# Performance work log

Hardware: AMD Instinct MI355X
Metric: run time of the kernel (lower is better)

Reference implementation:

```python
import jax, jax.numpy as jnp
import numpy as np

B, N, F, H1, H2, NC = 1024, 64, 1024, 256, 128, 128
ALPHA = 0.2   # LeakyReLU slope
BN_EPS = 1e-5


def setup_inputs() -> dict:
    key = jax.random.key(0)
    ks = jax.random.split(key, 20)
    d = {}
    d["x"] = jax.random.normal(ks[0], (B, 1, F), dtype=jnp.float32)
    d["neighbor"] = jax.random.normal(ks[1], (B, N, 1, F), dtype=jnp.float32)
    # GraphAttn layer 1 params
    d["W1"] = jax.random.normal(ks[2], (H1, F), dtype=jnp.float32) / np.sqrt(F)
    d["b1"] = jnp.zeros((H1,), dtype=jnp.float32)
    d["a11"] = jax.random.normal(ks[3], (H1,), dtype=jnp.float32) / np.sqrt(H1)
    d["a12"] = jax.random.normal(ks[4], (H1,), dtype=jnp.float32) / np.sqrt(H1)
    d["g1"] = jnp.ones((), dtype=jnp.float32)   # BatchNorm1d(1) weight (scalar)
    d["be1"] = jnp.zeros((), dtype=jnp.float32)  # BatchNorm1d(1) bias
    # GraphAttn layer 2 params
    d["W2"] = jax.random.normal(ks[5], (H2, H1), dtype=jnp.float32) / np.sqrt(H1)
    d["b2"] = jnp.zeros((H2,), dtype=jnp.float32)
    d["a21"] = jax.random.normal(ks[6], (H2,), dtype=jnp.float32) / np.sqrt(H2)
    d["a22"] = jax.random.normal(ks[7], (H2,), dtype=jnp.float32) / np.sqrt(H2)
    d["g2"] = jnp.ones((), dtype=jnp.float32)
    d["be2"] = jnp.zeros((), dtype=jnp.float32)
    # final classifier
    d["Wl"] = jax.random.normal(ks[8], (NC, H2), dtype=jnp.float32) / np.sqrt(H2)
    d["bl"] = jnp.zeros((NC,), dtype=jnp.float32)
    return d


def _l2norm_c(t):
    # torch nf.normalize default: p=2, dim=1 -> here the singleton channel axis (-2)
    n = jnp.sqrt(jnp.sum(t * t, axis=-2, keepdims=True))
    return t / jnp.maximum(n, 1e-12)


def _gat_layer(x, nb, W, b, a_self, a_nb):
    # x: [B,1,Fin], nb: [B,N,1,Fin]
    xh = jnp.einsum('bcf,hf->bch', x, W) + b        # [B,1,H]
    nbh = jnp.einsum('bncf,hf->bnch', nb, W) + b    # [B,N,1,H]
    # att1(x[i]) + att2(neighbor[i]) -> scores over N (C==1 squeezed)
    s = (jnp.einsum('bch,h->bc', xh, a_self)[:, None, :]
         + jnp.einsum('bnch,h->bnc', nbh, a_nb))[..., 0]   # [B,N]
    A = jax.nn.softmax(jax.nn.leaky_relu(s, ALPHA), axis=1)  # softmax over neighbors
    out = jnp.einsum('bn,bnch->bch', A, nbh)        # [B,1,H]
    return out, nbh


def _bn_relu(t, g, b, axes):
    # BatchNorm1d(1) in training mode: stats over all non-channel dims of the tensor
    m = jnp.mean(t, axis=axes, keepdims=True)
    v = jnp.mean(jnp.square(t - m), axis=axes, keepdims=True)
    return jax.nn.relu(g * (t - m) * jax.lax.rsqrt(v + BN_EPS) + b)


def reference(x, neighbor, W1, b1, a11, a12, g1, be1,
              W2, b2, a21, a22, g2, be2, Wl, bl):
    x = _l2norm_c(x)
    nb = _l2norm_c(neighbor)
    x, nb = _gat_layer(x, nb, W1, b1, a11, a12)
    # acvt1 applied to x [B,1,H1] (stats over B,H) and to each neighbor tensor
    # [N,1,H1] separately (per-sample stats -> axes (1,3) of [B,N,1,H1])
    x = _bn_relu(x, g1, be1, axes=(0, 2))
    nb = _bn_relu(nb, g1, be1, axes=(1, 3))
    x, nb = _gat_layer(x, nb, W2, b2, a21, a22)
    x = _bn_relu(x, g2, be2, axes=(0, 2))
    # Flatten -> Dropout(p=0) -> Linear
    logits = jnp.einsum('bh,ch->bc', x.reshape(x.shape[0], -1), Wl) + bl
    return logits
```

## Files before the change

### kernel.cpp

```cpp
#include <hip/hip_runtime.h>
#include <hip/hip_bf16.h>

#define B_    1024
#define N_    64
#define F_    1024
#define H1_   256
#define H2_   128
#define NC_   128
#define ALPHA 0.2f
#define BN_EPS 1e-5f

typedef __attribute__((ext_vector_type(4))) float  f32x4;
typedef __attribute__((ext_vector_type(8))) __bf16 bf16x8;
typedef __attribute__((ext_vector_type(4))) __bf16 bf16x4;

__device__ inline float sign_ref(float v) {
    float s = copysignf(1.0f, v);
    return (fabsf(v) >= 1e-12f) ? s : v * 1e12f;
}

__device__ inline float blk_reduce(float v, float* buf) {
    #pragma unroll
    for (int o = 32; o > 0; o >>= 1) v += __shfl_xor(v, o, 64);
    __syncthreads();
    const int wave = threadIdx.x >> 6, lane = threadIdx.x & 63;
    if (lane == 0) buf[wave] = v;
    __syncthreads();
    float r = 0.f;
    if (threadIdx.x == 0) {
        const int nw = blockDim.x >> 6;
        for (int i = 0; i < nw; ++i) r += buf[i];
    }
    return r;
}

__global__ __launch_bounds__(256) void k_prep(
    const float* __restrict__ W1, const float* __restrict__ W2,
    const float* __restrict__ b1, const float* __restrict__ a11,
    const float* __restrict__ b2, const float* __restrict__ a21,
    __bf16* __restrict__ W1b, __bf16* __restrict__ W2b,
    float* __restrict__ w1a, float* __restrict__ w2a, float* __restrict__ cscal)
{
    __shared__ float rbuf[8];
    const int blk = blockIdx.x, tid = threadIdx.x;
    if (blk < 256) {
        const int i0 = blk * 1024 + tid * 4;
        float4 v = *(const float4*)(W1 + i0);
        bf16x4 p = { (__bf16)v.x, (__bf16)v.y, (__bf16)v.z, (__bf16)v.w };
        *(bf16x4*)(W1b + i0) = p;
    } else if (blk < 288) {
        const int i0 = (blk - 256) * 1024 + tid * 4;
        float4 v = *(const float4*)(W2 + i0);
        bf16x4 p = { (__bf16)v.x, (__bf16)v.y, (__bf16)v.z, (__bf16)v.w };
        *(bf16x4*)(W2b + i0) = p;
    } else if (blk < 292) {
        const int f = (blk - 288) * 256 + tid;
        float s = 0.f;
        for (int h = 0; h < H1_; ++h) s += W1[h * F_ + f] * a11[h];
        w1a[f] = s;
    } else if (blk == 292) {
        float s = 0.f;
        for (int h = 0; h < H2_; ++h) s += W2[h * H1_ + tid] * a21[h];
        w2a[tid] = s;
    } else {
        float v1 = b1[tid] * a11[tid];
        float v2 = (tid < H2_) ? b2[tid] * a21[tid] : 0.f;
        float r1 = blk_reduce(v1, rbuf);
        float r2 = blk_reduce(v2, rbuf);
        if (tid == 0) { cscal[0] = r1; cscal[1] = r2; }
    }
}

__global__ __launch_bounds__(256) void k_sself1(
    const float* __restrict__ x, const float* __restrict__ w1a,
    const float* __restrict__ cscal, float* __restrict__ sself1)
{
    __shared__ float rbuf[8];
    const int b = blockIdx.x, tid = threadIdx.x;
    const float* xb = x + (size_t)b * F_;
    float p = 0.f;
    for (int i = tid; i < F_; i += 256) p += sign_ref(xb[i]) * w1a[i];
    float r = blk_reduce(p, rbuf);
    if (tid == 0) sself1[b] = r + cscal[0];
}

template<int BN, int MODE>
__global__ __launch_bounds__(256, 1) void k_gemm(
    const float* __restrict__ A, const int K,
    const __bf16* __restrict__ Bw, const float* __restrict__ bias,
    const float* __restrict__ alpha, const float* __restrict__ beta,
    const int rshift, float* __restrict__ C)
{
    constexpr int BM = 128, BK = 64;
    constexpr int WN = BN / 2;
    constexpr int NF = WN / 16;
    constexpr int MF = 4;
    constexpr int LDA = BK + 8;
    __shared__ __bf16 As[BM][LDA];
    __shared__ __bf16 Bs[BN][LDA];

    const int tid = threadIdx.x;
    const int wave = tid >> 6, lane = tid & 63;
    const int wm = wave & 1, wn = wave >> 1;
    const int rowin = lane & 15, kq = lane >> 4;
    const size_t m0 = (size_t)blockIdx.x * BM;

    f32x4 acc[MF][NF] = {};

    for (int k0 = 0; k0 < K; k0 += BK) {
        {
            const int cq = tid & 15;
            const int r0 = tid >> 4;
            const float* Ap = A + m0 * K + k0 + cq * 4;
            #pragma unroll
            for (int rr = 0; rr < BM / 16; ++rr) {
                const int r = r0 + rr * 16;
                float4 v = *(const float4*)(Ap + (size_t)r * K);
                float4 t;
                if (MODE == 0) {
                    t.x = sign_ref(v.x); t.y = sign_ref(v.y);
                    t.z = sign_ref(v.z); t.w = sign_ref(v.w);
                } else {
                    const int g = (int)((m0 + r) >> rshift);
                    const float al = alpha[g], bb = beta[g];
                    t.x = fmaxf(fmaf(al, v.x, bb), 0.f);
                    t.y = fmaxf(fmaf(al, v.y, bb), 0.f);
                    t.z = fmaxf(fmaf(al, v.z, bb), 0.f);
                    t.w = fmaxf(fmaf(al, v.w, bb), 0.f);
                }
                bf16x4 p = { (__bf16)t.x, (__bf16)t.y, (__bf16)t.z, (__bf16)t.w };
                *(bf16x4*)&As[r][cq * 4] = p;
            }
        }
        {
            const int cq = tid & 7;
            const int r0 = tid >> 3;
            const __bf16* Bp = Bw + k0 + cq * 8;
            #pragma unroll
            for (int rr = 0; rr < BN / 32; ++rr) {
                const int r = r0 + rr * 32;
                *(bf16x8*)&Bs[r][cq * 8] = *(const bf16x8*)(Bp + (size_t)r * K);
            }
        }
        __syncthreads();
        #pragma unroll
        for (int ks = 0; ks < 2; ++ks) {
            bf16x8 af[MF], bv[NF];
            #pragma unroll
            for (int mi = 0; mi < MF; ++mi)
                af[mi] = *(const bf16x8*)&As[wm * 64 + mi * 16 + rowin][ks * 32 + kq * 8];
            #pragma unroll
            for (int ni = 0; ni < NF; ++ni)
                bv[ni] = *(const bf16x8*)&Bs[wn * WN + ni * 16 + rowin][ks * 32 + kq * 8];
            #pragma unroll
            for (int mi = 0; mi < MF; ++mi)
                #pragma unroll
                for (int ni = 0; ni < NF; ++ni)
                    acc[mi][ni] = __builtin_amdgcn_mfma_f32_16x16x32_bf16(
                        af[mi], bv[ni], acc[mi][ni], 0, 0, 0);
        }
        __syncthreads();
    }
    const int cr0 = (lane >> 4) * 4, cc = lane & 15;
    #pragma unroll
    for (int ni = 0; ni < NF; ++ni) {
        const int col = wn * WN + ni * 16 + cc;
        const float bs = bias[col];
        #pragma unroll
        for (int mi = 0; mi < MF; ++mi) {
            #pragma unroll
            for (int i = 0; i < 4; ++i) {
                const size_t row = m0 + wm * 64 + mi * 16 + cr0 + i;
                C[row * BN + col] = acc[mi][ni][i] + bs;
            }
        }
    }
}

__global__ __launch_bounds__(256) void k_agg1(
    const float* __restrict__ nbh1, const float* __restrict__ sself1,
    const float* __restrict__ a12, const float* __restrict__ g1p,
    const float* __restrict__ be1p, float* __restrict__ out1,
    float* __restrict__ alpha1, float* __restrict__ beta1)
{
    __shared__ float tile[N_ * H1_];
    __shared__ float a12s[H1_];
    __shared__ float sv[N_];
    __shared__ float rbuf[8];
    const int b = blockIdx.x, tid = threadIdx.x;
    const float* src = nbh1 + (size_t)b * N_ * H1_;
    for (int i = tid; i < N_ * H1_ / 4; i += 256)
        ((float4*)tile)[i] = ((const float4*)src)[i];
    a12s[tid] = a12[tid];
    __syncthreads();
    {
        const int n = tid >> 2, q = tid & 3;
        float p = 0.f;
        #pragma unroll 4
        for (int i = 0; i < 64; ++i) {
            const int h = q * 64 + ((i + tid) & 63);
            p += tile[n * H1_ + h] * a12s[h];
        }
        p += __shfl_xor(p, 1); p += __shfl_xor(p, 2);
        if (q == 0) {
            float s = sself1[b] + p;
            sv[n] = s > 0.f ? s : ALPHA * s;
        }
    }
    __syncthreads();
    if (tid < 64) {
        float s = sv[tid], m = s;
        #pragma unroll
        for (int o = 1; o < 64; o <<= 1) m = fmaxf(m, __shfl_xor(m, o));
        float e = __expf(s - m), t = e;
        #pragma unroll
        for (int o = 1; o < 64; o <<= 1) t += __shfl_xor(t, o);
        sv[tid] = e / t;
    }
    __syncthreads();
    float acc = 0.f, ss = 0.f, sq = 0.f;
    for (int n2 = 0; n2 < N_; ++n2) {
        const float v = tile[n2 * H1_ + tid];
        acc += sv[n2] * v;
        ss += v; sq += v * v;
    }
    out1[(size_t)b * H1_ + tid] = acc;
    const float rs = blk_reduce(ss, rbuf);
    const float rq = blk_reduce(sq, rbuf);
    if (tid == 0) {
        const float inv = 1.f / (float)(N_ * H1_);
        const float mean = rs * inv, var = rq * inv - mean * mean;
        const float a = (*g1p) * rsqrtf(var + BN_EPS);
        alpha1[b] = a; beta1[b] = (*be1p) - a * mean;
    }
}

__global__ __launch_bounds__(256) void k_agg2(
    const float* __restrict__ nbh2, const float* __restrict__ sself2,
    const float* __restrict__ a22, float* __restrict__ out2)
{
    __shared__ float tile[N_ * H2_];
    __shared__ float a22s[H2_];
    __shared__ float sv[N_];
    const int b = blockIdx.x, tid = threadIdx.x;
    const float* src = nbh2 + (size_t)b * N_ * H2_;
    for (int i = tid; i < N_ * H2_ / 4; i += 256)
        ((float4*)tile)[i] = ((const float4*)src)[i];
    if (tid < H2_) a22s[tid] = a22[tid];
    __syncthreads();
    {
        const int n = tid >> 2, q = tid & 3;
        float p = 0.f;
        #pragma unroll 4
        for (int i = 0; i < 32; ++i) {
            const int h = q * 32 + ((i + tid) & 31);
            p += tile[n * H2_ + h] * a22s[h];
        }
        p += __shfl_xor(p, 1); p += __shfl_xor(p, 2);
        if (q == 0) {
            float s = sself2[b] + p;
            sv[n] = s > 0.f ? s : ALPHA * s;
        }
    }
    __syncthreads();
    if (tid < 64) {
        float s = sv[tid], m = s;
        #pragma unroll
        for (int o = 1; o < 64; o <<= 1) m = fmaxf(m, __shfl_xor(m, o));
        float e = __expf(s - m), t = e;
        #pragma unroll
        for (int o = 1; o < 64; o <<= 1) t += __shfl_xor(t, o);
        sv[tid] = e / t;
    }
    __syncthreads();
    if (tid < H2_) {
        float acc = 0.f;
        for (int n2 = 0; n2 < N_; ++n2) acc += sv[n2] * tile[n2 * H2_ + tid];
        out2[(size_t)b * H2_ + tid] = acc;
    }
}

__global__ __launch_bounds__(256) void k_bnred(
    const float* __restrict__ src, const int n,
    float* __restrict__ psum, float* __restrict__ psq)
{
    __shared__ float rbuf[8];
    float s = 0.f, q = 0.f;
    for (int i = blockIdx.x * 256 + threadIdx.x; i < n; i += 64 * 256) {
        const float v = src[i]; s += v; q += v * v;
    }
    const float rs = blk_reduce(s, rbuf);
    const float rq = blk_reduce(q, rbuf);
    if (threadIdx.x == 0) { psum[blockIdx.x] = rs; psq[blockIdx.x] = rq; }
}

__global__ void k_bnfin(
    const float* __restrict__ psum, const float* __restrict__ psq, const float n,
    const float* __restrict__ gp, const float* __restrict__ bep,
    float* __restrict__ axbx)
{
    const int tid = threadIdx.x;
    float s = psum[tid], q = psq[tid];
    #pragma unroll
    for (int o = 32; o > 0; o >>= 1) { s += __shfl_xor(s, o); q += __shfl_xor(q, o); }
    if (tid == 0) {
        const float mean = s / n, var = q / n - mean * mean;
        const float a = (*gp) * rsqrtf(var + BN_EPS);
        axbx[0] = a; axbx[1] = (*bep) - a * mean;
    }
}

__global__ __launch_bounds__(256) void k_sself2(
    const float* __restrict__ out1, const float* __restrict__ axbx,
    const float* __restrict__ w2a, const float* __restrict__ cscal,
    float* __restrict__ sself2)
{
    __shared__ float rbuf[8];
    const int b = blockIdx.x, tid = threadIdx.x;
    const float ax = axbx[0], bx = axbx[1];
    const float v = out1[(size_t)b * H1_ + tid];
    const float x2 = fmaxf(fmaf(ax, v, bx), 0.f);
    float r = blk_reduce(x2 * w2a[tid], rbuf);
    if (tid == 0) sself2[b] = r + cscal[1];
}

__global__ __launch_bounds__(128) void k_final(
    const float* __restrict__ out2, const float* __restrict__ axbx2,
    const float* __restrict__ Wl, const float* __restrict__ bl,
    float* __restrict__ logits)
{
    __shared__ float xr[H2_];
    __shared__ float Ws[NC_][H2_ + 1];
    const int b = blockIdx.x, tid = threadIdx.x;
    const float ax = axbx2[0], bx = axbx2[1];
    xr[tid] = fmaxf(fmaf(ax, out2[(size_t)b * H2_ + tid], bx), 0.f);
    for (int i = tid; i < NC_ * H2_ / 4; i += 128) {
        float4 v = ((const float4*)Wl)[i];
        const int r = i >> 5, c = (i & 31) * 4;
        Ws[r][c] = v.x; Ws[r][c + 1] = v.y; Ws[r][c + 2] = v.z; Ws[r][c + 3] = v.w;
    }
    __syncthreads();
    float acc = bl[tid];
    #pragma unroll 4
    for (int h = 0; h < H2_; ++h) acc += xr[h] * Ws[tid][h];
    logits[(size_t)b * NC_ + tid] = acc;
}

extern "C" void kernel_launch(void* const* d_in, const int* in_sizes, int n_in,
                              void* d_out, int out_size, void* d_ws, size_t ws_size,
                              hipStream_t stream)
{
    const float* x   = (const float*)d_in[0];
    const float* nb  = (const float*)d_in[1];
    const float* W1  = (const float*)d_in[2];
    const float* b1  = (const float*)d_in[3];
    const float* a11 = (const float*)d_in[4];
    const float* a12 = (const float*)d_in[5];
    const float* g1  = (const float*)d_in[6];
    const float* be1 = (const float*)d_in[7];
    const float* W2  = (const float*)d_in[8];
    const float* b2  = (const float*)d_in[9];
    const float* a21 = (const float*)d_in[10];
    const float* a22 = (const float*)d_in[11];
    const float* g2  = (const float*)d_in[12];
    const float* be2 = (const float*)d_in[13];
    const float* Wl  = (const float*)d_in[14];
    const float* bl  = (const float*)d_in[15];
    float* logits = (float*)d_out;

    size_t off = 0;
    auto alc = [&](size_t bytes) {
        void* p = (char*)d_ws + off;
        off = (off + bytes + 255) & ~(size_t)255;
        return p;
    };
    __bf16* W1b   = (__bf16*)alc((size_t)H1_ * F_ * 2);
    __bf16* W2b   = (__bf16*)alc((size_t)H2_ * H1_ * 2);
    float* w1a    = (float*)alc(F_ * 4);
    float* w2a    = (float*)alc(H1_ * 4);
    float* cscal  = (float*)alc(2 * 4);
    float* sself1 = (float*)alc(B_ * 4);
    float* sself2 = (float*)alc(B_ * 4);
    float* alpha1 = (float*)alc(B_ * 4);
    float* beta1  = (float*)alc(B_ * 4);
    float* psum   = (float*)alc(64 * 4);
    float* psq    = (float*)alc(64 * 4);
    float* axbx1  = (float*)alc(2 * 4);
    float* axbx2  = (float*)alc(2 * 4);
    float* out1   = (float*)alc((size_t)B_ * H1_ * 4);
    float* out2   = (float*)alc((size_t)B_ * H2_ * 4);
    float* nbh1   = (float*)alc((size_t)B_ * N_ * H1_ * 4);
    float* nbh2   = (float*)alc((size_t)B_ * N_ * H2_ * 4);

    k_prep<<<294, 256, 0, stream>>>(W1, W2, b1, a11, b2, a21, W1b, W2b, w1a, w2a, cscal);
    k_sself1<<<B_, 256, 0, stream>>>(x, w1a, cscal, sself1);
    k_gemm<256, 0><<<(B_ * N_) / 128, 256, 0, stream>>>(
        nb, F_, W1b, b1, nullptr, nullptr, 0, nbh1);
    k_agg1<<<B_, 256, 0, stream>>>(nbh1, sself1, a12, g1, be1, out1, alpha1, beta1);
    k_bnred<<<64, 256, 0, stream>>>(out1, B_ * H1_, psum, psq);
    k_bnfin<<<1, 64, 0, stream>>>(psum, psq, (float)(B_ * H1_), g1, be1, axbx1);
    k_sself2<<<B_, 256, 0, stream>>>(out1, axbx1, w2a, cscal, sself2);
    k_gemm<128, 1><<<(B_ * N_) / 128, 256, 0, stream>>>(
        nbh1, H1_, W2b, b2, alpha1, beta1, 6, nbh2);
    k_agg2<<<B_, 256, 0, stream>>>(nbh2, sself2, a22, out2);
    k_bnred<<<64, 256, 0, stream>>>(out2, B_ * H2_, psum, psq);
    k_bnfin<<<1, 64, 0, stream>>>(psum, psq, (float)(B_ * H2_), g2, be2, axbx2);
    k_final<<<B_, 128, 0, stream>>>(out2, axbx2, Wl, bl, logits);
}
```

Baseline: 518.0 us.

## Eliminate second-layer neighbor GEMM via algebraic reassociation and store nbh1 in bf16

The second GAT layer's per-neighbor GEMM is dropped. Attention scores come from a precomputed W2ᵀa22 vector, and the softmax-weighted sum of BN-ReLU'd nbh1 rows is taken first, then multiplied by W2 once per sample inside k_agg2. The first GEMM now writes nbh1 as bf16 through an LDS-staged coalesced epilogue and loads B tiles with global_load_lds into a swizzled layout, halving intermediate traffic. The BN-finalize kernels are folded into their consumers, which cuts launches. Storing nbh1 in bf16 adds rounding error to both layers.

```diff
diff --git a/kernel.cpp b/kernel.cpp
--- a/kernel.cpp
+++ b/kernel.cpp
@@ -1,5 +1,6 @@
 #include <hip/hip_runtime.h>
 #include <hip/hip_bf16.h>
+#include <stdint.h>
 
 #define B_    1024
 #define N_    64
@@ -19,6 +20,14 @@
     return (fabsf(v) >= 1e-12f) ? s : v * 1e12f;
 }
 
+__device__ __forceinline__ void gload_lds16(const void* g, void* l) {
+    auto gp = reinterpret_cast<const __attribute__((address_space(1))) void*>(
+        reinterpret_cast<uintptr_t>(g));
+    auto lp = reinterpret_cast<__attribute__((address_space(3))) void*>(
+        reinterpret_cast<uintptr_t>(l));
+    __builtin_amdgcn_global_load_lds(gp, lp, 16, 0, 0);
+}
+
 __device__ inline float blk_reduce(float v, float* buf) {
     #pragma unroll
     for (int o = 32; o > 0; o >>= 1) v += __shfl_xor(v, o, 64);
@@ -37,9 +46,12 @@
 __global__ __launch_bounds__(256) void k_prep(
     const float* __restrict__ W1, const float* __restrict__ W2,
     const float* __restrict__ b1, const float* __restrict__ a11,
-    const float* __restrict__ b2, const float* __restrict__ a21,
+    const float* __restrict__ a12, const float* __restrict__ b2,
+    const float* __restrict__ a21, const float* __restrict__ a22,
     __bf16* __restrict__ W1b, __bf16* __restrict__ W2b,
-    float* __restrict__ w1a, float* __restrict__ w2a, float* __restrict__ cscal)
+    float* __restrict__ w1a, float* __restrict__ w1a12,
+    float* __restrict__ w2a, float* __restrict__ w2a22,
+    float* __restrict__ cscal)
 {
     __shared__ float rbuf[8];
     const int blk = blockIdx.x, tid = threadIdx.x;
@@ -55,19 +67,27 @@
         *(bf16x4*)(W2b + i0) = p;
     } else if (blk < 292) {
         const int f = (blk - 288) * 256 + tid;
-        float s = 0.f;
-        for (int h = 0; h < H1_; ++h) s += W1[h * F_ + f] * a11[h];
-        w1a[f] = s;
+        float s1 = 0.f, s2 = 0.f;
+        for (int h = 0; h < H1_; ++h) {
+            const float w = W1[h * F_ + f];
+            s1 += w * a11[h]; s2 += w * a12[h];
+        }
+        w1a[f] = s1; w1a12[f] = s2;
     } else if (blk == 292) {
-        float s = 0.f;
-        for (int h = 0; h < H2_; ++h) s += W2[h * H1_ + tid] * a21[h];
-        w2a[tid] = s;
+        float s1 = 0.f, s2 = 0.f;
+        for (int h = 0; h < H2_; ++h) {
+            const float w = W2[h * H1_ + tid];
+            s1 += w * a21[h]; s2 += w * a22[h];
+        }
+        w2a[tid] = s1; w2a22[tid] = s2;
     } else {
         float v1 = b1[tid] * a11[tid];
         float v2 = (tid < H2_) ? b2[tid] * a21[tid] : 0.f;
+        float v3 = (tid < H2_) ? b2[tid] * a22[tid] : 0.f;
         float r1 = blk_reduce(v1, rbuf);
         float r2 = blk_reduce(v2, rbuf);
-        if (tid == 0) { cscal[0] = r1; cscal[1] = r2; }
+        float r3 = blk_reduce(v3, rbuf);
+        if (tid == 0) { cscal[0] = r1; cscal[1] = r2; cscal[2] = r3; }
     }
 }
 
@@ -84,20 +104,16 @@
     if (tid == 0) sself1[b] = r + cscal[0];
 }
 
-template<int BN, int MODE>
-__global__ __launch_bounds__(256, 1) void k_gemm(
-    const float* __restrict__ A, const int K,
-    const __bf16* __restrict__ Bw, const float* __restrict__ bias,
-    const float* __restrict__ alpha, const float* __restrict__ beta,
-    const int rshift, float* __restrict__ C)
-{
-    constexpr int BM = 128, BK = 64;
-    constexpr int WN = BN / 2;
-    constexpr int NF = WN / 16;
-    constexpr int MF = 4;
+__global__ __launch_bounds__(256, 1) void k_gemm1(
+    const float* __restrict__ A, const __bf16* __restrict__ Bw,
+    const float* __restrict__ bias, __bf16* __restrict__ C)
+{
+    constexpr int BM = 128, BN = 256, BK = 64, K = F_;
     constexpr int LDA = BK + 8;
-    __shared__ __bf16 As[BM][LDA];
-    __shared__ __bf16 Bs[BN][LDA];
+    __shared__ __attribute__((aligned(16))) char smem[BM * LDA * 2 + BN * BK * 2];
+    __bf16* As = (__bf16*)smem;
+    __bf16* Bs = (__bf16*)(smem + BM * LDA * 2);
+    __bf16* Cs = Bs;
 
     const int tid = threadIdx.x;
     const int wave = tid >> 6, lane = tid & 63;
@@ -105,107 +121,101 @@
     const int rowin = lane & 15, kq = lane >> 4;
     const size_t m0 = (size_t)blockIdx.x * BM;
 
-    f32x4 acc[MF][NF] = {};
+    f32x4 acc[4][8] = {};
+
+    const int cqA = tid & 15, r0A = tid >> 4;
+    const float* Abase = A + m0 * K + cqA * 4;
 
     for (int k0 = 0; k0 < K; k0 += BK) {
-        {
-            const int cq = tid & 15;
-            const int r0 = tid >> 4;
-            const float* Ap = A + m0 * K + k0 + cq * 4;
+        #pragma unroll
+        for (int it = 0; it < 8; ++it) {
+            const int s = it * 256 + tid;
+            const int r = s >> 3;
+            const int c8 = (s & 7) ^ (r & 7);
+            gload_lds16(Bw + (size_t)r * K + k0 + c8 * 8, Bs + s * 8);
+        }
+        #pragma unroll
+        for (int rr = 0; rr < 8; ++rr) {
+            const int r = r0A + rr * 16;
+            float4 v = *(const float4*)(Abase + (size_t)r * K + k0);
+            bf16x4 p = { (__bf16)sign_ref(v.x), (__bf16)sign_ref(v.y),
+                         (__bf16)sign_ref(v.z), (__bf16)sign_ref(v.w) };
+            *(bf16x4*)&As[r * LDA + cqA * 4] = p;
+        }
+        __syncthreads();
+        #pragma unroll
+        for (int ks = 0; ks < 2; ++ks) {
+            bf16x8 af[4], bv[8];
             #pragma unroll
-            for (int rr = 0; rr < BM / 16; ++rr) {
-                const int r = r0 + rr * 16;
-                float4 v = *(const float4*)(Ap + (size_t)r * K);
-                float4 t;
-                if (MODE == 0) {
-                    t.x = sign_ref(v.x); t.y = sign_ref(v.y);
-                    t.z = sign_ref(v.z); t.w = sign_ref(v.w);
-                } else {
-                    const int g = (int)((m0 + r) >> rshift);
-                    const float al = alpha[g], bb = beta[g];
-                    t.x = fmaxf(fmaf(al, v.x, bb), 0.f);
-                    t.y = fmaxf(fmaf(al, v.y, bb), 0.f);
-                    t.z = fmaxf(fmaf(al, v.z, bb), 0.f);
-                    t.w = fmaxf(fmaf(al, v.w, bb), 0.f);
-                }
-                bf16x4 p = { (__bf16)t.x, (__bf16)t.y, (__bf16)t.z, (__bf16)t.w };
-                *(bf16x4*)&As[r][cq * 4] = p;
+            for (int mi = 0; mi < 4; ++mi)
+                af[mi] = *(const bf16x8*)&As[(wm * 64 + mi * 16 + rowin) * LDA + ks * 32 + kq * 8];
+            #pragma unroll
+            for (int ni = 0; ni < 8; ++ni) {
+                const int r = wn * 128 + ni * 16 + rowin;
+                const int c = (ks * 4 + kq) ^ (r & 7);
+                bv[ni] = *(const bf16x8*)&Bs[(r * 8 + c) * 8];
             }
-        }
-        {
-            const int cq = tid & 7;
-            const int r0 = tid >> 3;
-            const __bf16* Bp = Bw + k0 + cq * 8;
             #pragma unroll
-            for (int rr = 0; rr < BN / 32; ++rr) {
-                const int r = r0 + rr * 32;
-                *(bf16x8*)&Bs[r][cq * 8] = *(const bf16x8*)(Bp + (size_t)r * K);
-            }
-        }
-        __syncthreads();
-        #pragma unroll
-        for (int ks = 0; ks < 2; ++ks) {
-            bf16x8 af[MF], bv[NF];
-            #pragma unroll
-            for (int mi = 0; mi < MF; ++mi)
-                af[mi] = *(const bf16x8*)&As[wm * 64 + mi * 16 + rowin][ks * 32 + kq * 8];
-            #pragma unroll
-            for (int ni = 0; ni < NF; ++ni)
-                bv[ni] = *(const bf16x8*)&Bs[wn * WN + ni * 16 + rowin][ks * 32 + kq * 8];
-            #pragma unroll
-            for (int mi = 0; mi < MF; ++mi)
+            for (int mi = 0; mi < 4; ++mi)
                 #pragma unroll
-                for (int ni = 0; ni < NF; ++ni)
+                for (int ni = 0; ni < 8; ++ni)
                     acc[mi][ni] = __builtin_amdgcn_mfma_f32_16x16x32_bf16(
                         af[mi], bv[ni], acc[mi][ni], 0, 0, 0);
         }
         __syncthreads();
     }
     const int cr0 = (lane >> 4) * 4, cc = lane & 15;
-    #pragma unroll
-    for (int ni = 0; ni < NF; ++ni) {
-        const int col = wn * WN + ni * 16 + cc;
-        const float bs = bias[col];
-        #pragma unroll
-        for (int mi = 0; mi < MF; ++mi) {
+    for (int half = 0; half < 2; ++half) {
+        if (wm == half) {
             #pragma unroll
-            for (int i = 0; i < 4; ++i) {
-                const size_t row = m0 + wm * 64 + mi * 16 + cr0 + i;
-                C[row * BN + col] = acc[mi][ni][i] + bs;
+            for (int ni = 0; ni < 8; ++ni) {
+                const int col = wn * 128 + ni * 16 + cc;
+                const float bs = bias[col];
+                #pragma unroll
+                for (int mi = 0; mi < 4; ++mi)
+                    #pragma unroll
+                    for (int i = 0; i < 4; ++i)
+                        Cs[(mi * 16 + cr0 + i) * 256 + col] =
+                            (__bf16)(acc[mi][ni][i] + bs);
             }
         }
+        __syncthreads();
+        #pragma unroll
+        for (int it = 0; it < 8; ++it) {
+            const int s = it * 256 + tid;
+            const size_t row = m0 + half * 64 + (s >> 5);
+            *(bf16x8*)(C + row * 256 + (s & 31) * 8) = *(const bf16x8*)&Cs[s * 8];
+        }
+        __syncthreads();
     }
 }
 
 __global__ __launch_bounds__(256) void k_agg1(
-    const float* __restrict__ nbh1, const float* __restrict__ sself1,
+    const __bf16* __restrict__ nbh1, const float* __restrict__ sself1,
     const float* __restrict__ a12, const float* __restrict__ g1p,
     const float* __restrict__ be1p, float* __restrict__ out1,
     float* __restrict__ alpha1, float* __restrict__ beta1)
 {
-    __shared__ float tile[N_ * H1_];
+    __shared__ __attribute__((aligned(16))) __bf16 tile[N_ * H1_];
     __shared__ float a12s[H1_];
     __shared__ float sv[N_];
     __shared__ float rbuf[8];
     const int b = blockIdx.x, tid = threadIdx.x;
-    const float* src = nbh1 + (size_t)b * N_ * H1_;
-    for (int i = tid; i < N_ * H1_ / 4; i += 256)
-        ((float4*)tile)[i] = ((const float4*)src)[i];
+    const __bf16* src = nbh1 + (size_t)b * N_ * H1_;
+    #pragma unroll
+    for (int it = 0; it < 8; ++it)
+        ((bf16x8*)tile)[it * 256 + tid] = ((const bf16x8*)src)[it * 256 + tid];
     a12s[tid] = a12[tid];
     __syncthreads();
     {
         const int n = tid >> 2, q = tid & 3;
         float p = 0.f;
-        #pragma unroll 4
         for (int i = 0; i < 64; ++i) {
             const int h = q * 64 + ((i + tid) & 63);
-            p += tile[n * H1_ + h] * a12s[h];
+            p += (float)tile[n * H1_ + h] * a12s[h];
         }
         p += __shfl_xor(p, 1); p += __shfl_xor(p, 2);
-        if (q == 0) {
-            float s = sself1[b] + p;
-            sv[n] = s > 0.f ? s : ALPHA * s;
-        }
+        if (q == 0) { float s = sself1[b] + p; sv[n] = s > 0.f ? s : ALPHA * s; }
     }
     __syncthreads();
     if (tid < 64) {
@@ -220,9 +230,8 @@
     __syncthreads();
     float acc = 0.f, ss = 0.f, sq = 0.f;
     for (int n2 = 0; n2 < N_; ++n2) {
-        const float v = tile[n2 * H1_ + tid];
-        acc += sv[n2] * v;
-        ss += v; sq += v * v;
+        const float v = (float)tile[n2 * H1_ + tid];
+        acc += sv[n2] * v; ss += v; sq += v * v;
     }
     out1[(size_t)b * H1_ + tid] = acc;
     const float rs = blk_reduce(ss, rbuf);
@@ -235,51 +244,6 @@
     }
 }
 
-__global__ __launch_bounds__(256) void k_agg2(
-    const float* __restrict__ nbh2, const float* __restrict__ sself2,
-    const float* __restrict__ a22, float* __restrict__ out2)
-{
-    __shared__ float tile[N_ * H2_];
-    __shared__ float a22s[H2_];
-    __shared__ float sv[N_];
-    const int b = blockIdx.x, tid = threadIdx.x;
-    const float* src = nbh2 + (size_t)b * N_ * H2_;
-    for (int i = tid; i < N_ * H2_ / 4; i += 256)
-        ((float4*)tile)[i] = ((const float4*)src)[i];
-    if (tid < H2_) a22s[tid] = a22[tid];
-    __syncthreads();
-    {
-        const int n = tid >> 2, q = tid & 3;
-        float p = 0.f;
-        #pragma unroll 4
-        for (int i = 0; i < 32; ++i) {
-            const int h = q * 32 + ((i + tid) & 31);
-            p += tile[n * H2_ + h] * a22s[h];
-        }
-        p += __shfl_xor(p, 1); p += __shfl_xor(p, 2);
-        if (q == 0) {
-            float s = sself2[b] + p;
-            sv[n] = s > 0.f ? s : ALPHA * s;
-        }
-    }
-    __syncthreads();
-    if (tid < 64) {
-        float s = sv[tid], m = s;
-        #pragma unroll
-        for (int o = 1; o < 64; o <<= 1) m = fmaxf(m, __shfl_xor(m, o));
-        float e = __expf(s - m), t = e;
-        #pragma unroll
-        for (int o = 1; o < 64; o <<= 1) t += __shfl_xor(t, o);
-        sv[tid] = e / t;
-    }
-    __syncthreads();
-    if (tid < H2_) {
-        float acc = 0.f;
-        for (int n2 = 0; n2 < N_; ++n2) acc += sv[n2] * tile[n2 * H2_ + tid];
-        out2[(size_t)b * H2_ + tid] = acc;
-    }
-}
-
 __global__ __launch_bounds__(256) void k_bnred(
     const float* __restrict__ src, const int n,
     float* __restrict__ psum, float* __restrict__ psq)
@@ -294,29 +258,27 @@
     if (threadIdx.x == 0) { psum[blockIdx.x] = rs; psq[blockIdx.x] = rq; }
 }
 
-__global__ void k_bnfin(
-    const float* __restrict__ psum, const float* __restrict__ psq, const float n,
-    const float* __restrict__ gp, const float* __restrict__ bep,
-    float* __restrict__ axbx)
-{
-    const int tid = threadIdx.x;
-    float s = psum[tid], q = psq[tid];
-    #pragma unroll
-    for (int o = 32; o > 0; o >>= 1) { s += __shfl_xor(s, o); q += __shfl_xor(q, o); }
-    if (tid == 0) {
-        const float mean = s / n, var = q / n - mean * mean;
-        const float a = (*gp) * rsqrtf(var + BN_EPS);
-        axbx[0] = a; axbx[1] = (*bep) - a * mean;
-    }
-}
-
 __global__ __launch_bounds__(256) void k_sself2(
-    const float* __restrict__ out1, const float* __restrict__ axbx,
-    const float* __restrict__ w2a, const float* __restrict__ cscal,
-    float* __restrict__ sself2)
+    const float* __restrict__ out1, const float* __restrict__ psum,
+    const float* __restrict__ psq, const float* __restrict__ gp,
+    const float* __restrict__ bep, const float* __restrict__ w2a,
+    const float* __restrict__ cscal, float* __restrict__ sself2)
 {
     __shared__ float rbuf[8];
+    __shared__ float axbx[2];
     const int b = blockIdx.x, tid = threadIdx.x;
+    if (tid < 64) {
+        float s = psum[tid], q = psq[tid];
+        #pragma unroll
+        for (int o = 32; o > 0; o >>= 1) { s += __shfl_xor(s, o); q += __shfl_xor(q, o); }
+        if (tid == 0) {
+            const float n = (float)(B_ * H1_);
+            const float mean = s / n, var = q / n - mean * mean;
+            const float a = (*gp) * rsqrtf(var + BN_EPS);
+            axbx[0] = a; axbx[1] = (*bep) - a * mean;
+        }
+    }
+    __syncthreads();
     const float ax = axbx[0], bx = axbx[1];
     const float v = out1[(size_t)b * H1_ + tid];
     const float x2 = fmaxf(fmaf(ax, v, bx), 0.f);
@@ -324,21 +286,107 @@
     if (tid == 0) sself2[b] = r + cscal[1];
 }
 
+__global__ __launch_bounds__(256) void k_agg2(
+    const __bf16* __restrict__ nbh1, const float* __restrict__ alpha1,
+    const float* __restrict__ beta1, const float* __restrict__ sself2,
+    const float* __restrict__ w2a22, const float* __restrict__ cscal,
+    const __bf16* __restrict__ W2b, const float* __restrict__ b2,
+    float* __restrict__ out2)
+{
+    __shared__ __attribute__((aligned(16))) __bf16 tile[N_ * H1_];
+    __shared__ float wv[H1_];
+    __shared__ float sv[N_];
+    __shared__ float g2s[H1_ + 8];
+    __shared__ float hpart[H2_];
+    const int b = blockIdx.x, tid = threadIdx.x;
+    const __bf16* src = nbh1 + (size_t)b * N_ * H1_;
+    #pragma unroll
+    for (int it = 0; it < 8; ++it)
+        ((bf16x8*)tile)[it * 256 + tid] = ((const bf16x8*)src)[it * 256 + tid];
+    wv[tid] = w2a22[tid];
+    const float al = alpha1[b], be = beta1[b];
+    __syncthreads();
+    {
+        const int n = tid >> 2, q = tid & 3;
+        float p = 0.f;
+        for (int i = 0; i < 64; ++i) {
+            const int h = q * 64 + ((i + tid) & 63);
+            const float v = (float)tile[n * H1_ + h];
+            p += fmaxf(fmaf(al, v, be), 0.f) * wv[h];
+        }
+        p += __shfl_xor(p, 1); p += __shfl_xor(p, 2);
+        if (q == 0) {
+            float s = sself2[b] + p + cscal[2];
+            sv[n] = s > 0.f ? s : ALPHA * s;
+        }
+    }
+    __syncthreads();
+    if (tid < 64) {
+        float s = sv[tid], m = s;
+        #pragma unroll
+        for (int o = 1; o < 64; o <<= 1) m = fmaxf(m, __shfl_xor(m, o));
+        float e = __expf(s - m), t = e;
+        #pragma unroll
+        for (int o = 1; o < 64; o <<= 1) t += __shfl_xor(t, o);
+        sv[tid] = e / t;
+    }
+    __syncthreads();
+    {
+        float g = 0.f;
+        for (int n2 = 0; n2 < N_; ++n2) {
+            const float v = (float)tile[n2 * H1_ + tid];
+            g += sv[n2] * fmaxf(fmaf(al, v, be), 0.f);
+        }
+        g2s[tid + (tid >> 5)] = g;
+    }
+    __syncthreads();
+    #pragma unroll 4
+    for (int j = 0; j < 16; ++j) {
+        const int idx = j * 256 + tid;
+        const int h = idx >> 5, k8 = idx & 31;
+        const bf16x8 w = ((const bf16x8*)W2b)[idx];
+        float p = 0.f;
+        #pragma unroll
+        for (int i = 0; i < 8; ++i) {
+            const int k = k8 * 8 + i;
+            p += (float)w[i] * g2s[k + (k >> 5)];
+        }
+        p += __shfl_xor(p, 1); p += __shfl_xor(p, 2); p += __shfl_xor(p, 4);
+        p += __shfl_xor(p, 8); p += __shfl_xor(p, 16);
+        if ((tid & 31) == 0) hpart[h] = p;
+    }
+    __syncthreads();
+    if (tid < H2_) out2[(size_t)b * H2_ + tid] = hpart[tid] + b2[tid];
+}
+
 __global__ __launch_bounds__(128) void k_final(
-    const float* __restrict__ out2, const float* __restrict__ axbx2,
-    const float* __restrict__ Wl, const float* __restrict__ bl,
-    float* __restrict__ logits)
+    const float* __restrict__ out2, const float* __restrict__ psum,
+    const float* __restrict__ psq, const float* __restrict__ gp,
+    const float* __restrict__ bep, const float* __restrict__ Wl,
+    const float* __restrict__ bl, float* __restrict__ logits)
 {
     __shared__ float xr[H2_];
     __shared__ float Ws[NC_][H2_ + 1];
+    __shared__ float axbx[2];
     const int b = blockIdx.x, tid = threadIdx.x;
-    const float ax = axbx2[0], bx = axbx2[1];
-    xr[tid] = fmaxf(fmaf(ax, out2[(size_t)b * H2_ + tid], bx), 0.f);
+    if (tid < 64) {
+        float s = psum[tid], q = psq[tid];
+        #pragma unroll
+        for (int o = 32; o > 0; o >>= 1) { s += __shfl_xor(s, o); q += __shfl_xor(q, o); }
+        if (tid == 0) {
+            const float n = (float)(B_ * H2_);
+            const float mean = s / n, var = q / n - mean * mean;
+            const float a = (*gp) * rsqrtf(var + BN_EPS);
+            axbx[0] = a; axbx[1] = (*bep) - a * mean;
+        }
+    }
     for (int i = tid; i < NC_ * H2_ / 4; i += 128) {
         float4 v = ((const float4*)Wl)[i];
         const int r = i >> 5, c = (i & 31) * 4;
         Ws[r][c] = v.x; Ws[r][c + 1] = v.y; Ws[r][c + 2] = v.z; Ws[r][c + 3] = v.w;
     }
+    __syncthreads();
+    xr[tid] = fmaxf(fmaf(axbx[0], out2[(size_t)b * H2_ + tid], axbx[1]), 0.f);
     __syncthreads();
     float acc = bl[tid];
     #pragma unroll 4
@@ -377,33 +425,31 @@
     __bf16* W1b   = (__bf16*)alc((size_t)H1_ * F_ * 2);
     __bf16* W2b   = (__bf16*)alc((size_t)H2_ * H1_ * 2);
     float* w1a    = (float*)alc(F_ * 4);
+    float* w1a12  = (float*)alc(F_ * 4);
     float* w2a    = (float*)alc(H1_ * 4);
-    float* cscal  = (float*)alc(2 * 4);
+    float* w2a22  = (float*)alc(H1_ * 4);
+    float* cscal  = (float*)alc(3 * 4);
     float* sself1 = (float*)alc(B_ * 4);
     float* sself2 = (float*)alc(B_ * 4);
     float* alpha1 = (float*)alc(B_ * 4);
     float* beta1  = (float*)alc(B_ * 4);
-    float* psum   = (float*)alc(64 * 4);
-    float* psq    = (float*)alc(64 * 4);
-    float* axbx1  = (float*)alc(2 * 4);
-    float* axbx2  = (float*)alc(2 * 4);
+    float* psum1  = (float*)alc(64 * 4);
+    float* psq1   = (float*)alc(64 * 4);
+    float* psum2  = (float*)alc(64 * 4);
+    float* psq2   = (float*)alc(64 * 4);
     float* out1   = (float*)alc((size_t)B_ * H1_ * 4);
     float* out2   = (float*)alc((size_t)B_ * H2_ * 4);
-    float* nbh1   = (float*)alc((size_t)B_ * N_ * H1_ * 4);
-    float* nbh2   = (float*)alc((size_t)B_ * N_ * H2_ * 4);
-
-    k_prep<<<294, 256, 0, stream>>>(W1, W2, b1, a11, b2, a21, W1b, W2b, w1a, w2a, cscal);
+    __bf16* nbh1  = (__bf16*)alc((size_t)B_ * N_ * H1_ * 2);
+
+    k_prep<<<294, 256, 0, stream>>>(W1, W2, b1, a11, a12, b2, a21, a22,
+                                    W1b, W2b, w1a, w1a12, w2a, w2a22, cscal);
     k_sself1<<<B_, 256, 0, stream>>>(x, w1a, cscal, sself1);
-    k_gemm<256, 0><<<(B_ * N_) / 128, 256, 0, stream>>>(
-        nb, F_, W1b, b1, nullptr, nullptr, 0, nbh1);
+    k_gemm1<<<(B_ * N_) / 128, 256, 0, stream>>>(nb, W1b, b1, nbh1);
     k_agg1<<<B_, 256, 0, stream>>>(nbh1, sself1, a12, g1, be1, out1, alpha1, beta1);
-    k_bnred<<<64, 256, 0, stream>>>(out1, B_ * H1_, psum, psq);
-    k_bnfin<<<1, 64, 0, stream>>>(psum, psq, (float)(B_ * H1_), g1, be1, axbx1);
-    k_sself2<<<B_, 256, 0, stream>>>(out1, axbx1, w2a, cscal, sself2);
-    k_gemm<128, 1><<<(B_ * N_) / 128, 256, 0, stream>>>(
-        nbh1, H1_, W2b, b2, alpha1, beta1, 6, nbh2);
-    k_agg2<<<B_, 256, 0, stream>>>(nbh2, sself2, a22, out2);
-    k_bnred<<<64, 256, 0, stream>>>(out2, B_ * H2_, psum, psq);
-    k_bnfin<<<1, 64, 0, stream>>>(psum, psq, (float)(B_ * H2_), g2, be2, axbx2);
-    k_final<<<B_, 128, 0, stream>>>(out2, axbx2, Wl, bl, logits);
-}
+    k_bnred<<<64, 256, 0, stream>>>(out1, B_ * H1_, psum1, psq1);
+    k_sself2<<<B_, 256, 0, stream>>>(out1, psum1, psq1, g1, be1, w2a, cscal, sself2);
+    k_agg2<<<B_, 256, 0, stream>>>(nbh1, alpha1, beta1, sself2, w2a22, cscal,
+                                   W2b, b2, out2);
+    k_bnred<<<64, 256, 0, stream>>>(out2, B_ * H2_, psum2, psq2);
+    k_final<<<B_, 128, 0, stream>>>(out2, psum2, psq2, g2, be2, Wl, bl, logits);
+}
```

Result: faster. 501.5 us (-3.2%).
